# Kernel tuning notes

Hardware: AMD Instinct MI355X
Metric: run time of the kernel (lower is better)

## Reference

```python
import jax, jax.numpy as jnp
import numpy as np

EPS = 1e-6
K = 20
NEG_SLOPE = 0.2

def knn_idx(x, k):
    # x: (B, D, N) flattened vector features; returns (B, N, k) neighbor indices
    inner = -2.0 * jnp.einsum('bdn,bdm->bnm', x, x)
    xx = jnp.sum(x * x, axis=1)  # (B, N)
    pd = -xx[:, :, None] - inner - xx[:, None, :]  # negative squared distance
    _, idx = jax.lax.top_k(pd, k)
    return idx

def get_graph_feature(x, k):
    # x: (B, C, 3, N) -> (B, 2C, 3, N, k) edge features (nbr - ctr, ctr)
    B, C, _, N = x.shape
    idx = knn_idx(x.reshape(B, C * 3, N), k)           # (B, N, k)
    feat = jnp.transpose(x, (0, 3, 1, 2))              # (B, N, C, 3)
    nb = jax.vmap(lambda f, i: f[i])(feat, idx)        # (B, N, k, C, 3)
    ctr = jnp.broadcast_to(feat[:, :, None], nb.shape)
    out = jnp.concatenate([nb - ctr, ctr], axis=3)     # (B, N, k, 2C, 3)
    return jnp.transpose(out, (0, 3, 4, 1, 2))

def vn_batchnorm(x, gamma, beta):
    # x: (B, C, 3, ...); BatchNorm (training stats) applied to vector norms
    norm = jnp.linalg.norm(x, axis=2) + EPS            # (B, C, ...)
    axes = (0,) + tuple(range(2, norm.ndim))
    mu = jnp.mean(norm, axis=axes, keepdims=True)
    var = jnp.var(norm, axis=axes, keepdims=True)
    shape = (1, -1) + (1,) * (norm.ndim - 2)
    nbn = (norm - mu) / jnp.sqrt(var + 1e-5) * gamma.reshape(shape) + beta.reshape(shape)
    return x / norm[:, :, None] * nbn[:, :, None]

def vn_linear_leakyrelu(x, w_feat, w_dir, gamma, beta):
    # x: (B, Cin, 3, ...) -> (B, Cout, 3, ...)
    p = jnp.einsum('oc,bc...->bo...', w_feat, x)
    p = vn_batchnorm(p, gamma, beta)
    d = jnp.einsum('oc,bc...->bo...', w_dir, x)
    dot = jnp.sum(p * d, axis=2, keepdims=True)
    dsq = jnp.sum(d * d, axis=2, keepdims=True)
    proj = p - (dot / (dsq + EPS)) * d
    return NEG_SLOPE * p + (1.0 - NEG_SLOPE) * jnp.where(dot >= 0, p, proj)

def _forward(x, w1, d1, g1, b1, w2, d2, g2, b2, w3, d3, g3, b3, w4, d4, g4, b4, w5, d5, g5, b5):
    h = jnp.transpose(x, (0, 2, 1))[:, None]           # (B, 1, 3, N)
    h = vn_linear_leakyrelu(get_graph_feature(h, K), w1, d1, g1, b1)
    x1 = jnp.mean(h, axis=-1)                          # mean_pool over k: (B, 21, 3, N)
    h = vn_linear_leakyrelu(get_graph_feature(x1, K), w2, d2, g2, b2)
    x2 = jnp.mean(h, axis=-1)                          # (B, 21, 3, N)
    h = vn_linear_leakyrelu(get_graph_feature(x2, K), w3, d3, g3, b3)
    x3 = jnp.mean(h, axis=-1)                          # (B, 42, 3, N)
    h = vn_linear_leakyrelu(get_graph_feature(x3, K), w4, d4, g4, b4)
    x4 = jnp.mean(h, axis=-1)                          # (B, 85, 3, N)
    cat = jnp.concatenate([x1, x2, x3, x4], axis=1)    # (B, 169, 3, N)
    return vn_linear_leakyrelu(cat, w5, d5, g5, b5)    # (B, 341, 3, N)

def setup_inputs():
    key = jax.random.key(0)
    B, N = 8, 1024
    d = {"x": jax.random.normal(key, (B, N, 3), dtype=jnp.float32)}
    feat_shapes = {"1": (21, 2), "2": (21, 42), "3": (42, 42), "4": (85, 84), "5": (341, 169)}
    dir_out = {"1": 21, "2": 21, "3": 42, "4": 85, "5": 1}  # conv5 shares nonlinearity -> 1 dir channel
    for i, (name, (co, ci)) in enumerate(feat_shapes.items()):
        k1, k2 = jax.random.split(jax.random.fold_in(key, i + 1))
        s = 1.0 / np.sqrt(ci)
        d["w" + name] = jax.random.uniform(k1, (co, ci), minval=-s, maxval=s, dtype=jnp.float32)
        d["d" + name] = jax.random.uniform(k2, (dir_out[name], ci), minval=-s, maxval=s, dtype=jnp.float32)
        d["g" + name] = jnp.ones((co,), dtype=jnp.float32)
        d["b" + name] = jnp.zeros((co,), dtype=jnp.float32)
    return d

def reference(x, w1, d1, g1, b1, w2, d2, g2, b2, w3, d3, g3, b3, w4, d4, g4, b4, w5, d5, g5, b5):
    return _forward(x, w1, d1, g1, b1, w2, d2, g2, b2, w3, d3, g3, b3, w4, d4, g4, b4, w5, d5, g5, b5)
```

## Files before the change

### kernel.cpp

```cpp
#include <hip/hip_runtime.h>
#include <math.h>

#define KNN 20
#define NS 0.2f
#define EPSV 1e-6f
#define QT 4
#define OT 8
#define TN 8
#define CROW 507
#define SSPLIT 8

struct F3 { float x, y, z; };

extern __shared__ __align__(16) float smem[];

__global__ void k_transpose(const float* __restrict__ x, float* __restrict__ xt,
                            float* __restrict__ xx, int B, int N) {
    int i = blockIdx.x * blockDim.x + threadIdx.x;
    if (i >= B * N) return;
    int b = i / N, n = i % N;
    const float* src = x + (size_t)(b * N + n) * 3;
    float* dst = xt + (size_t)b * 3 * N + n;
    float s0 = src[0], s1 = src[1], s2 = src[2];
    dst[0] = s0;
    dst[(size_t)N] = s1;
    dst[(size_t)2 * N] = s2;
    float s = 0.f;
    s += s0 * s0;
    s += s1 * s1;
    s += s2 * s2;
    xx[i] = s;
}

__global__ void k_knn_mm(
                         const float* __restrict__ Xn, const float* __restrict__ xx,
                         int* __restrict__ idx, int N, int D,
                         long batchStride, long sliceOff, int qPerBlock,
                         const float* __restrict__ Xp, const float* __restrict__ W,
                         const float* __restrict__ Dw,
                         float* __restrict__ U, float* __restrict__ V,
                         float* __restrict__ UD, float* __restrict__ VD,
                         int C, int Co, int CoP, int TILE,
                         int rowStride, int colOff, int mmBlocks) {
    float* sm = smem;
    int tid = threadIdx.x;

    if ((int)blockIdx.x < mmBlocks) {
        const int CP = C * CoP;
        float* wts = sm;
        float* xs = sm + 4 * CP;
        int bn0 = blockIdx.x * TILE;
        int C3 = C * 3;

        int npad = CoP - Co;
        if (npad) {
            for (int t = tid; t < 4 * C * npad; t += 256) {
                int q = t / npad, oo = Co + t % npad;
                int mat = q / C, c = q % C;
                wts[mat * CP + c * CoP + oo] = 0.f;
            }
        }
        int twoCC = 2 * C * Co;
        for (int t = tid; t < twoCC; t += 256) {
            int o = t / (2 * C), c = t % (2 * C);
            float w = W[t], dw = Dw[t];
            if (c < C) {
                wts[c * CoP + o] = w;
                wts[2 * CP + c * CoP + o] = dw;
            } else {
                wts[CP + (c - C) * CoP + o] = w;
                wts[3 * CP + (c - C) * CoP + o] = dw;
            }
        }
        for (int t = tid; t < TILE * C3; t += 256) {
            int p = t / C3, cc = t % C3;
            xs[t] = Xp[(size_t)(bn0 + p) * rowStride + colOff + cc];
        }
        __syncthreads();
        for (int t = tid; t < CP; t += 256) {
            wts[CP + t] -= wts[t];
            wts[3 * CP + t] -= wts[2 * CP + t];
        }
        __syncthreads();

        int GPP = CoP >> 2;
        int items = TILE * GPP;
        for (int e = tid; e < items; e += 256) {
            int p = e / GPP, og = e - p * GPP;
            int o0 = og * 4;
            const float* xr = xs + p * C3;

            float aU[4][3], aV[4][3], aDu[4][3], aDv[4][3];
#pragma unroll
            for (int i = 0; i < 4; ++i)
#pragma unroll
                for (int j = 0; j < 3; ++j) {
                    aU[i][j] = 0.f; aV[i][j] = 0.f; aDu[i][j] = 0.f; aDv[i][j] = 0.f;
                }

            for (int c = 0; c < C; ++c) {
                float x0 = xr[c * 3], x1 = xr[c * 3 + 1], x2 = xr[c * 3 + 2];
                const float* wp = wts + c * CoP + o0;
                float4 wa4 = *(const float4*)(wp);
                float4 wb4 = *(const float4*)(wp + CP);
                float4 da4 = *(const float4*)(wp + 2 * CP);
                float4 db4 = *(const float4*)(wp + 3 * CP);
                float wav[4] = {wa4.x, wa4.y, wa4.z, wa4.w};
                float wbv[4] = {wb4.x, wb4.y, wb4.z, wb4.w};
                float dav[4] = {da4.x, da4.y, da4.z, da4.w};
                float dbv[4] = {db4.x, db4.y, db4.z, db4.w};
#pragma unroll
                for (int i = 0; i < 4; ++i) {
                    aU[i][0] += wav[i] * x0; aU[i][1] += wav[i] * x1; aU[i][2] += wav[i] * x2;
                    aV[i][0] += wbv[i] * x0; aV[i][1] += wbv[i] * x1; aV[i][2] += wbv[i] * x2;
                    aDu[i][0] += dav[i] * x0; aDu[i][1] += dav[i] * x1; aDu[i][2] += dav[i] * x2;
                    aDv[i][0] += dbv[i] * x0; aDv[i][1] += dbv[i] * x1; aDv[i][2] += dbv[i] * x2;
                }
            }

            size_t base = ((size_t)(bn0 + p) * Co + o0) * 3;
#pragma unroll
            for (int i = 0; i < 4; ++i) {
                int o = o0 + i;
                if (o < Co) {
                    size_t off = base + (size_t)i * 3;
                    U[off] = aU[i][0]; U[off + 1] = aU[i][1]; U[off + 2] = aU[i][2];
                    V[off] = aV[i][0]; V[off + 1] = aV[i][1]; V[off + 2] = aV[i][2];
                    UD[off] = aDu[i][0]; UD[off + 1] = aDu[i][1]; UD[off + 2] = aDu[i][2];
                    VD[off] = aDv[i][0]; VD[off + 1] = aDv[i][1]; VD[off + 2] = aDv[i][2];
                }
            }
        }
        return;
    }

    int kb = (int)blockIdx.x - mmBlocks;
    int qbpb = N / qPerBlock;
    int b = kb / qbpb;
    int qbase = (kb - b * qbpb) * qPerBlock;
    int lane = tid & 63;
    int wave = tid >> 6;

    float* qf = sm;
    float* pdb = sm + 128 * QT;

    const float* Xb = Xn + (size_t)b * batchStride + sliceOff;
    const float* xxb = xx + (size_t)b * N;

    for (int q0 = qbase; q0 < qbase + qPerBlock; q0 += QT) {
        for (int t = tid; t < QT * D; t += 256) {
            int d = t >> 2, q = t & 3;
            qf[d * QT + q] = Xb[(size_t)d * N + (q0 + q)];
        }
        __syncthreads();

        float a0x = 0.f, a0y = 0.f, a0z = 0.f, a0w = 0.f;
        float a1x = 0.f, a1y = 0.f, a1z = 0.f, a1w = 0.f;
        float a2x = 0.f, a2y = 0.f, a2z = 0.f, a2w = 0.f;
        float a3x = 0.f, a3y = 0.f, a3z = 0.f, a3w = 0.f;

        const float* mbase = Xb + 4 * tid;
#pragma unroll 3
        for (int d = 0; d < D; ++d) {
            float4 xm = *(const float4*)(mbase + (size_t)d * N);
            float4 qv = *(const float4*)(qf + d * QT);
            a0x += qv.x * xm.x; a0y += qv.x * xm.y; a0z += qv.x * xm.z; a0w += qv.x * xm.w;
            a1x += qv.y * xm.x; a1y += qv.y * xm.y; a1z += qv.y * xm.z; a1w += qv.y * xm.w;
            a2x += qv.z * xm.x; a2y += qv.z * xm.y; a2z += qv.z * xm.z; a2w += qv.z * xm.w;
            a3x += qv.w * xm.x; a3y += qv.w * xm.y; a3z += qv.w * xm.z; a3w += qv.w * xm.w;
        }

        {
            float4 m2 = *(const float4*)(xxb + 4 * tid);
            float4 qn = *(const float4*)(xxb + q0);
            float4 v;
            v.x = 2.f * a0x - qn.x - m2.x; v.y = 2.f * a0y - qn.x - m2.y;
            v.z = 2.f * a0z - qn.x - m2.z; v.w = 2.f * a0w - qn.x - m2.w;
            *(float4*)(pdb + 0 * 1024 + 4 * tid) = v;
            v.x = 2.f * a1x - qn.y - m2.x; v.y = 2.f * a1y - qn.y - m2.y;
            v.z = 2.f * a1z - qn.y - m2.z; v.w = 2.f * a1w - qn.y - m2.w;
            *(float4*)(pdb + 1 * 1024 + 4 * tid) = v;
            v.x = 2.f * a2x - qn.z - m2.x; v.y = 2.f * a2y - qn.z - m2.y;
            v.z = 2.f * a2z - qn.z - m2.z; v.w = 2.f * a2w - qn.z - m2.w;
            *(float4*)(pdb + 2 * 1024 + 4 * tid) = v;
            v.x = 2.f * a3x - qn.w - m2.x; v.y = 2.f * a3y - qn.w - m2.y;
            v.z = 2.f * a3z - qn.w - m2.z; v.w = 2.f * a3w - qn.w - m2.w;
            *(float4*)(pdb + 3 * 1024 + 4 * tid) = v;
        }
        __syncthreads();

        unsigned long long key[16];
#pragma unroll
        for (int t = 0; t < 16; ++t) {
            unsigned u = __float_as_uint(pdb[wave * 1024 + t * 64 + lane]);
            u ^= (unsigned)((int)u >> 31) | 0x80000000u;
            unsigned lo = (unsigned)(1023 - t * 64) - (unsigned)lane;
            key[t] = ((unsigned long long)u << 32) | (unsigned long long)lo;
        }

#define CE(a, b)                                        \
        {                                               \
            unsigned long long ka = key[a], kb2 = key[b]; \
            bool sw = ka < kb2;                         \
            key[a] = sw ? kb2 : ka;                     \
            key[b] = sw ? ka : kb2;                     \
        }
        CE(0,1) CE(2,3) CE(4,5) CE(6,7) CE(8,9) CE(10,11) CE(12,13) CE(14,15)
        CE(0,2) CE(1,3) CE(4,6) CE(5,7) CE(8,10) CE(9,11) CE(12,14) CE(13,15)
        CE(1,2) CE(5,6) CE(9,10) CE(13,14)
        CE(0,4) CE(1,5) CE(2,6) CE(3,7) CE(8,12) CE(9,13) CE(10,14) CE(11,15)
        CE(2,4) CE(3,5) CE(10,12) CE(11,13)
        CE(1,2) CE(3,4) CE(5,6) CE(9,10) CE(11,12) CE(13,14)
        CE(0,8) CE(1,9) CE(2,10) CE(3,11) CE(4,12) CE(5,13) CE(6,14) CE(7,15)
        CE(4,8) CE(5,9) CE(6,10) CE(7,11)
        CE(2,4) CE(3,5) CE(6,8) CE(7,9) CE(10,12) CE(11,13)
        CE(1,2) CE(3,4) CE(5,6) CE(7,8) CE(9,10) CE(11,12) CE(13,14)
#undef CE

        __syncthreads();
        unsigned long long* kl = (unsigned long long*)(pdb + wave * 1024);
#pragma unroll
        for (int t = 8; t < 16; ++t) kl[(t - 8) * 64 + lane] = key[t];
        int nspill = 0;

        long outBase = ((long)b * N + q0 + wave) * KNN;
        for (int it = 0; it < KNN; ++it) {
            unsigned myh = (unsigned)(key[0] >> 32);
            unsigned mylo = (unsigned)(key[0] & 0xFFFFFFFFull);
            unsigned bh = myh;
#pragma unroll
            for (int off = 32; off >= 1; off >>= 1) {
                unsigned oh = __shfl_xor(bh, off, 64);
                if (oh > bh) bh = oh;
            }
            unsigned long long mask = __ballot(myh == bh);
            unsigned ml;
            if (__popcll(mask) == 1) {
                int src = (int)(__ffsll((long long)mask) - 1);
                ml = __shfl(mylo, src, 64);
            } else {
                unsigned cand = (myh == bh) ? mylo : 0u;
#pragma unroll
                for (int off = 32; off >= 1; off >>= 1) {
                    unsigned oc = __shfl_xor(cand, off, 64);
                    if (oc > cand) cand = oc;
                }
                ml = cand;
            }
            int bi = 1023 - (int)(ml & 1023u);
            if (lane == 0) idx[outBase + it] = bi;
            if ((bi & 63) == lane) {
                key[0] = key[1]; key[1] = key[2]; key[2] = key[3]; key[3] = key[4];
                key[4] = key[5]; key[5] = key[6]; key[6] = key[7];
                int sidx = nspill < 8 ? nspill : 7;
                unsigned long long nv = kl[sidx * 64 + lane];
                key[7] = (nspill < 8) ? nv : 0ull;
                nspill++;
            }
        }
        __syncthreads();
    }
}

__global__ void k_matmul_pair_lds(const float* __restrict__ X, const float* __restrict__ W,
                                  const float* __restrict__ Dw,
                                  float* __restrict__ U, float* __restrict__ V,
                                  float* __restrict__ UD, float* __restrict__ VD,
                                  int C, int Co, int CoP, int TILE,
                                  int rowStride, int colOff) {
    const int CP = C * CoP;
    float* wts = smem;
    float* xs = smem + 4 * CP;

    int tid = threadIdx.x;
    int bn0 = blockIdx.x * TILE;
    int C3 = C * 3;

    int npad = CoP - Co;
    if (npad) {
        for (int t = tid; t < 4 * C * npad; t += 256) {
            int q = t / npad, oo = Co + t % npad;
            int mat = q / C, c = q % C;
            wts[mat * CP + c * CoP + oo] = 0.f;
        }
    }
    int twoCC = 2 * C * Co;
    for (int t = tid; t < twoCC; t += 256) {
        int o = t / (2 * C), c = t % (2 * C);
        float w = W[t], dw = Dw[t];
        if (c < C) {
            wts[c * CoP + o] = w;
            wts[2 * CP + c * CoP + o] = dw;
        } else {
            wts[CP + (c - C) * CoP + o] = w;
            wts[3 * CP + (c - C) * CoP + o] = dw;
        }
    }
    for (int t = tid; t < TILE * C3; t += 256) {
        int p = t / C3, cc = t % C3;
        xs[t] = X[(size_t)(bn0 + p) * rowStride + colOff + cc];
    }
    __syncthreads();
    for (int t = tid; t < CP; t += 256) {
        wts[CP + t] -= wts[t];
        wts[3 * CP + t] -= wts[2 * CP + t];
    }
    __syncthreads();

    int GPP = CoP >> 2;
    int items = TILE * GPP;
    for (int e = tid; e < items; e += 256) {
        int p = e / GPP, og = e - p * GPP;
        int o0 = og * 4;
        const float* xr = xs + p * C3;

        float aU[4][3], aV[4][3], aDu[4][3], aDv[4][3];
#pragma unroll
        for (int i = 0; i < 4; ++i)
#pragma unroll
            for (int j = 0; j < 3; ++j) {
                aU[i][j] = 0.f; aV[i][j] = 0.f; aDu[i][j] = 0.f; aDv[i][j] = 0.f;
            }

        for (int c = 0; c < C; ++c) {
            float x0 = xr[c * 3], x1 = xr[c * 3 + 1], x2 = xr[c * 3 + 2];
            const float* wp = wts + c * CoP + o0;
            float4 wa4 = *(const float4*)(wp);
            float4 wb4 = *(const float4*)(wp + CP);
            float4 da4 = *(const float4*)(wp + 2 * CP);
            float4 db4 = *(const float4*)(wp + 3 * CP);
            float wav[4] = {wa4.x, wa4.y, wa4.z, wa4.w};
            float wbv[4] = {wb4.x, wb4.y, wb4.z, wb4.w};
            float dav[4] = {da4.x, da4.y, da4.z, da4.w};
            float dbv[4] = {db4.x, db4.y, db4.z, db4.w};
#pragma unroll
            for (int i = 0; i < 4; ++i) {
                aU[i][0] += wav[i] * x0; aU[i][1] += wav[i] * x1; aU[i][2] += wav[i] * x2;
                aV[i][0] += wbv[i] * x0; aV[i][1] += wbv[i] * x1; aV[i][2] += wbv[i] * x2;
                aDu[i][0] += dav[i] * x0; aDu[i][1] += dav[i] * x1; aDu[i][2] += dav[i] * x2;
                aDv[i][0] += dbv[i] * x0; aDv[i][1] += dbv[i] * x1; aDv[i][2] += dbv[i] * x2;
            }
        }

        size_t base = ((size_t)(bn0 + p) * Co + o0) * 3;
#pragma unroll
        for (int i = 0; i < 4; ++i) {
            int o = o0 + i;
            if (o < Co) {
                size_t off = base + (size_t)i * 3;
                U[off] = aU[i][0]; U[off + 1] = aU[i][1]; U[off + 2] = aU[i][2];
                V[off] = aV[i][0]; V[off + 1] = aV[i][1]; V[off + 2] = aV[i][2];
                UD[off] = aDu[i][0]; UD[off + 1] = aDu[i][1]; UD[off + 2] = aDu[i][2];
                VD[off] = aDv[i][0]; VD[off + 1] = aDv[i][1]; VD[off + 2] = aDv[i][2];
            }
        }
    }
}

__global__ void k_stats_edge_det(const float* __restrict__ U, const float* __restrict__ V,
                                 const int* __restrict__ idx, float* __restrict__ partials,
                                 int N, int Co, int BN) {
    int o = blockIdx.x;
    int s = blockIdx.y;
    int tid = threadIdx.x;
    int P = BN / SSPLIT;
    int g0 = s * P;

    __shared__ float Ush[3072];
    __shared__ float r1[256], r2[256];

    for (int t = tid; t < P; t += 256) {
        F3 u3 = *(const F3*)(U + ((size_t)(g0 + t) * Co + o) * 3);
        Ush[t * 3 + 0] = u3.x;
        Ush[t * 3 + 1] = u3.y;
        Ush[t * 3 + 2] = u3.z;
    }
    __syncthreads();

    float s1 = 0.f, s2 = 0.f;
    for (int pl = tid; pl < P; pl += 256) {
        int g = g0 + pl;
        F3 v3 = *(const F3*)(V + ((size_t)g * Co + o) * 3);
        float v0 = v3.x, v1 = v3.y, v2 = v3.z;
        const int* ip = idx + (size_t)g * KNN;
        for (int kk = 0; kk < KNN; ++kk) {
            const float* Ur = Ush + ip[kk] * 3;
            float p0 = Ur[0] + v0;
            float p1 = Ur[1] + v1;
            float p2 = Ur[2] + v2;
            float nm = sqrtf(p0 * p0 + p1 * p1 + p2 * p2) + EPSV;
            s1 += nm;
            s2 += nm * nm;
        }
    }
    r1[tid] = s1; r2[tid] = s2;
    __syncthreads();
    for (int st = 128; st > 0; st >>= 1) {
        if (tid < st) { r1[tid] += r1[tid + st]; r2[tid] += r2[tid + st]; }
        __syncthreads();
    }
    if (tid == 0) {
        partials[(o * SSPLIT + s) * 2] = r1[0];
        partials[(o * SSPLIT + s) * 2 + 1] = r2[0];
    }
}

__global__ void k_final_fused(const float* __restrict__ U, const float* __restrict__ V,
                              const float* __restrict__ UD, const float* __restrict__ VD,
                              const int* __restrict__ idx, const float* __restrict__ partials,
                              const float* __restrict__ gamma, const float* __restrict__ beta,
                              float* __restrict__ catp, float* __restrict__ catn,
                              float* __restrict__ xx,
                              int N, int Co, int colOff, float cnt, int doSq) {
    int b = blockIdx.y;
    int n0 = blockIdx.x * TN;
    int tid = threadIdx.x;
    int CC = Co * 3;

    __shared__ float tile[TN * 255];
    __shared__ float muS[85], invS[85];

    for (int o = tid; o < Co; o += 256) {
        float s1 = 0.f, s2 = 0.f;
        for (int s = 0; s < SSPLIT; ++s) {
            s1 += partials[(o * SSPLIT + s) * 2];
            s2 += partials[(o * SSPLIT + s) * 2 + 1];
        }
        float mu = s1 / cnt;
        float var = s2 / cnt - mu * mu;
        muS[o] = mu;
        invS[o] = rsqrtf(var + 1e-5f);
    }
    __syncthreads();

    const float invk = 1.f / (float)KNN;
    int items = TN * Co;
    for (int e = tid; e < items; e += 256) {
        int nl = e / Co, o = e - nl * Co;
        int n = n0 + nl;
        float mu = muS[o], inv = invS[o];
        float gmm = gamma[o], bt = beta[o];

        size_t ctr = ((size_t)(b * N + n) * Co + o) * 3;
        F3 vc = *(const F3*)(V + ctr);
        F3 wc = *(const F3*)(VD + ctr);
        float v0 = vc.x, v1 = vc.y, v2 = vc.z;
        float w0 = wc.x, w1 = wc.y, w2 = wc.z;
        const int* ip = idx + ((size_t)b * N + n) * KNN;

        float a0 = 0.f, a1 = 0.f, a2 = 0.f;
        for (int kk = 0; kk < KNN; ++kk) {
            int m = ip[kk];
            size_t nb = ((size_t)(b * N + m) * Co + o) * 3;
            F3 un = *(const F3*)(U + nb);
            F3 dn = *(const F3*)(UD + nb);
            float p0 = un.x + v0;
            float p1 = un.y + v1;
            float p2 = un.z + v2;
            float nm = sqrtf(p0 * p0 + p1 * p1 + p2 * p2) + EPSV;
            float nbn = (nm - mu) * inv * gmm + bt;
            float sc = nbn / nm;
            p0 *= sc; p1 *= sc; p2 *= sc;
            float d0 = dn.x + w0;
            float d1 = dn.y + w1;
            float d2 = dn.z + w2;
            float dot = p0 * d0 + p1 * d1 + p2 * d2;
            if (dot >= 0.f) {
                a0 += p0; a1 += p1; a2 += p2;
            } else {
                float f = dot / (d0 * d0 + d1 * d1 + d2 * d2 + EPSV);
                a0 += NS * p0 + (1.f - NS) * (p0 - f * d0);
                a1 += NS * p1 + (1.f - NS) * (p1 - f * d1);
                a2 += NS * p2 + (1.f - NS) * (p2 - f * d2);
            }
        }
        tile[nl * CC + o * 3 + 0] = a0 * invk;
        tile[nl * CC + o * 3 + 1] = a1 * invk;
        tile[nl * CC + o * 3 + 2] = a2 * invk;
    }
    __syncthreads();

    for (int t = tid; t < TN * CC; t += 256) {
        int nl = t / CC, c = t - nl * CC;
        catp[(size_t)(b * N + n0 + nl) * CROW + colOff + c] = tile[nl * CC + c];
    }
    for (int t = tid; t < TN * CC; t += 256) {
        int c = t >> 3, nl = t & (TN - 1);
        catn[(size_t)b * CROW * N + (size_t)(colOff + c) * N + n0 + nl] = tile[nl * CC + c];
    }
    if (doSq && tid < TN) {
        const float* row = tile + tid * CC;
        float s = 0.f;
        for (int c = 0; c < CC; ++c) {
            float v = row[c];
            s += v * v;
        }
        xx[(size_t)b * N + n0 + tid] = s;
    }
}

__global__ void k_matmul_plain(const float* __restrict__ X, const float* __restrict__ W,
                               const float* __restrict__ Dw,
                               float* __restrict__ U, float* __restrict__ Ud,
                               int N, int Cin, int Cout, long batchStride, long sliceOff) {
    int ot = blockIdx.y;
    int b = blockIdx.z;
    int tid = threadIdx.x;
    int n = blockIdx.x * 512 + 2 * tid;

    const float* Wp; float* Up; int CoutE; int o0;
    if (ot == (int)gridDim.y - 1) {
        Wp = Dw; Up = Ud; CoutE = 1; o0 = 0;
    } else {
        Wp = W; Up = U; CoutE = Cout; o0 = ot * OT;
    }

    __shared__ __align__(16) float wsm[OT][176];
    for (int t = tid; t < OT * Cin; t += 256) {
        int oo = t / Cin, c = t % Cin;
        int o = o0 + oo;
        wsm[oo][c] = (o < CoutE) ? Wp[(size_t)o * Cin + c] : 0.f;
    }
    __syncthreads();

    const float* Xp = X + (size_t)b * batchStride + sliceOff + n;
    float au[OT][3][2];
#pragma unroll
    for (int oo = 0; oo < OT; ++oo)
#pragma unroll
        for (int j = 0; j < 3; ++j) {
            au[oo][j][0] = 0.f; au[oo][j][1] = 0.f;
        }

    int c = 0;
    for (; c + 4 <= Cin; c += 4) {
        float2 xv[4][3];
#pragma unroll
        for (int cc = 0; cc < 4; ++cc)
#pragma unroll
            for (int j = 0; j < 3; ++j)
                xv[cc][j] = *(const float2*)(Xp + ((size_t)(c + cc) * 3 + j) * N);
#pragma unroll
        for (int oo = 0; oo < OT; ++oo) {
            float4 w4 = *(const float4*)&wsm[oo][c];
            float wv[4] = {w4.x, w4.y, w4.z, w4.w};
#pragma unroll
            for (int j = 0; j < 3; ++j) {
#pragma unroll
                for (int cc = 0; cc < 4; ++cc) {
                    au[oo][j][0] += wv[cc] * xv[cc][j].x;
                    au[oo][j][1] += wv[cc] * xv[cc][j].y;
                }
            }
        }
    }
    for (; c < Cin; ++c) {
        float2 xv[3];
#pragma unroll
        for (int j = 0; j < 3; ++j)
            xv[j] = *(const float2*)(Xp + ((size_t)c * 3 + j) * N);
#pragma unroll
        for (int oo = 0; oo < OT; ++oo) {
            float wv = wsm[oo][c];
#pragma unroll
            for (int j = 0; j < 3; ++j) {
                au[oo][j][0] += wv * xv[j].x;
                au[oo][j][1] += wv * xv[j].y;
            }
        }
    }
#pragma unroll
    for (int oo = 0; oo < OT; ++oo) {
        int o = o0 + oo;
        if (o < CoutE) {
#pragma unroll
            for (int j = 0; j < 3; ++j) {
                float2 st; st.x = au[oo][j][0]; st.y = au[oo][j][1];
                *(float2*)&Up[(((size_t)b * CoutE + o) * 3 + j) * N + n] = st;
            }
        }
    }
}

__global__ void k_stats_plain_det(const float* __restrict__ U, float* __restrict__ mv,
                                  int N, int Cout, int BN, float cnt) {
    int o = blockIdx.x;
    int tid = threadIdx.x;
    float s1 = 0.f, s2 = 0.f;
    for (int g = tid; g < BN; g += 256) {
        int b = g / N, n = g % N;
        const float* Ub = U + (((size_t)b * Cout + o) * 3) * N;
        float p0 = Ub[n], p1 = Ub[(size_t)N + n], p2 = Ub[(size_t)2 * N + n];
        float nm = sqrtf(p0 * p0 + p1 * p1 + p2 * p2) + EPSV;
        s1 += nm;
        s2 += nm * nm;
    }
    __shared__ float r1[256], r2[256];
    r1[tid] = s1; r2[tid] = s2;
    __syncthreads();
    for (int st = 128; st > 0; st >>= 1) {
        if (tid < st) { r1[tid] += r1[tid + st]; r2[tid] += r2[tid + st]; }
        __syncthreads();
    }
    if (tid == 0) {
        float mu = r1[0] / cnt;
        float var = r2[0] / cnt - mu * mu;
        mv[2 * o] = mu;
        mv[2 * o + 1] = rsqrtf(var + 1e-5f);
    }
}

__global__ void k_final_plain(const float* __restrict__ U, const float* __restrict__ Dv,
                              const float* __restrict__ mv,
                              const float* __restrict__ gamma, const float* __restrict__ beta,
                              float* __restrict__ out, int N, int Cout) {
    int b = blockIdx.z, o = blockIdx.y, tid = threadIdx.x;
    int n = blockIdx.x * 256 + tid;
    float mu = mv[2 * o];
    float inv = mv[2 * o + 1];
    float g = gamma[o], bt = beta[o];

    const float* Ub = U + (((size_t)b * Cout + o) * 3) * N;
    float p0 = Ub[n], p1 = Ub[(size_t)N + n], p2 = Ub[(size_t)2 * N + n];
    float nm = sqrtf(p0 * p0 + p1 * p1 + p2 * p2) + EPSV;
    float nbn = (nm - mu) * inv * g + bt;
    float sc = nbn / nm;
    p0 *= sc; p1 *= sc; p2 *= sc;

    float d0 = Dv[((size_t)b * 3 + 0) * N + n];
    float d1 = Dv[((size_t)b * 3 + 1) * N + n];
    float d2 = Dv[((size_t)b * 3 + 2) * N + n];
    float dot = p0 * d0 + p1 * d1 + p2 * d2;
    float o0, o1, o2;
    if (dot >= 0.f) {
        o0 = p0; o1 = p1; o2 = p2;
    } else {
        float f = dot / (d0 * d0 + d1 * d1 + d2 * d2 + EPSV);
        o0 = NS * p0 + (1.f - NS) * (p0 - f * d0);
        o1 = NS * p1 + (1.f - NS) * (p1 - f * d1);
        o2 = NS * p2 + (1.f - NS) * (p2 - f * d2);
    }
    size_t ob = (((size_t)b * Cout + o) * 3) * N + n;
    out[ob] = o0;
    out[ob + (size_t)N] = o1;
    out[ob + (size_t)2 * N] = o2;
}

extern "C" void kernel_launch(void* const* d_in, const int* in_sizes, int n_in,
                              void* d_out, int out_size, void* d_ws, size_t ws_size,
                              hipStream_t stream) {
    (void)in_sizes; (void)n_in; (void)out_size; (void)ws_size;
    const int B = 8, N = 1024;

    const float* x = (const float*)d_in[0];
    const float* W[5]; const float* Dw[5]; const float* G[5]; const float* Bt[5];
    for (int l = 0; l < 5; ++l) {
        W[l]  = (const float*)d_in[1 + 4 * l];
        Dw[l] = (const float*)d_in[2 + 4 * l];
        G[l]  = (const float*)d_in[3 + 4 * l];
        Bt[l] = (const float*)d_in[4 + 4 * l];
    }

    float* ws = (float*)d_ws;
    size_t off = 0;
    float* xt = ws + off;     off += (size_t)B * 3 * N;
    int* idx = (int*)(ws + off); off += (size_t)B * N * KNN;
    float* catp = ws + off;   off += (size_t)B * N * CROW;
    float* catn = ws + off;   off += (size_t)B * N * CROW;
    float* Up = ws + off;     off += (size_t)B * N * 85 * 3;
    float* Vp = ws + off;     off += (size_t)B * N * 85 * 3;
    float* UDp = ws + off;    off += (size_t)B * N * 85 * 3;
    float* VDp = ws + off;    off += (size_t)B * N * 85 * 3;
    float* U5 = ws + off;     off += (size_t)B * 341 * 3 * N;
    float* d5buf = ws + off;  off += (size_t)B * 3 * N;
    float* xx = ws + off;     off += (size_t)B * N;
    float* partials = ws + off; off += (size_t)341 * SSPLIT * 2;
    float* mv = ws + off;     off += 2 * 341;

    k_transpose<<<(B * N + 255) / 256, 256, 0, stream>>>(x, xt, xx, B, N);

    const int Cin_[4]  = {1, 21, 21, 42};
    const int Cout_[4] = {21, 21, 42, 85};
    const int inOff_[4] = {-1, 0, 21, 42};
    const int outOff_[4] = {0, 21, 42, 84};
    const int Tile_[4] = {32, 32, 16, 8};

    const int BN = B * N;
    const size_t KNN_LDS = (size_t)(128 * QT + QT * 1024) * sizeof(float);

    for (int l = 0; l < 4; ++l) {
        int C = Cin_[l], Co = Cout_[l];
        int D = C * 3;
        int CoP = (Co + 3) & ~3;
        int TILE = Tile_[l];

        const float* Xn; long bs, so;
        if (inOff_[l] < 0) { Xn = xt; bs = (long)3 * N; so = 0; }
        else { Xn = catn; bs = (long)CROW * N; so = (long)inOff_[l] * 3 * N; }

        const float* Xp; int rs, co;
        if (inOff_[l] < 0) { Xp = x; rs = 3; co = 0; }
        else { Xp = catp; rs = CROW; co = inOff_[l] * 3; }

        size_t mmNeed = (size_t)(4 * C * CoP + TILE * C * 3) * sizeof(float);

        if (l < 3) {
            int mmB = BN / TILE;
            int knnB = BN / 8;
            size_t smemB = mmNeed > KNN_LDS ? mmNeed : KNN_LDS;
            k_knn_mm<<<mmB + knnB, 256, smemB, stream>>>(
                Xn, xx, idx, N, D, bs, so, 8,
                Xp, W[l], Dw[l], Up, Vp, UDp, VDp, C, Co, CoP, TILE, rs, co, mmB);
        } else {
            k_knn_mm<<<BN / 4, 256, KNN_LDS, stream>>>(
                Xn, xx, idx, N, D, bs, so, 4,
                Xp, W[l], Dw[l], Up, Vp, UDp, VDp, C, Co, CoP, TILE, rs, co, 0);
            k_matmul_pair_lds<<<BN / TILE, 256, mmNeed, stream>>>(
                Xp, W[l], Dw[l], Up, Vp, UDp, VDp, C, Co, CoP, TILE, rs, co);
        }

        dim3 gst(Co, SSPLIT);
        k_stats_edge_det<<<gst, 256, 0, stream>>>(Up, Vp, idx, partials, N, Co, BN);

        int doSq = (l < 3) ? 1 : 0;
        dim3 gf(N / TN, B);
        k_final_fused<<<gf, 256, 0, stream>>>(
            Up, Vp, UDp, VDp, idx, partials, G[l], Bt[l],
            catp, catn, xx, N, Co, outOff_[l] * 3,
            (float)((size_t)BN * KNN), doSq);
    }

    {
        long bs = (long)CROW * N, so = 0;
        dim3 gm5(N / 512, (341 + OT - 1) / OT + 1, B);
        k_matmul_plain<<<gm5, 256, 0, stream>>>(catn, W[4], Dw[4], U5, d5buf,
                                                N, 169, 341, bs, so);
        k_stats_plain_det<<<341, 256, 0, stream>>>(U5, mv, N, 341, BN, (float)BN);
        dim3 gs5(N / 256, 341, B);
        k_final_plain<<<gs5, 256, 0, stream>>>(U5, d5buf, mv, G[4], Bt[4],
                                               (float*)d_out, N, 341);
    }
}
```

Before: 653.1 us.

## Fuse layer-4 matmul into kNN kernel via output-channel-chunked weight staging

Layer 4 now runs its pairwise matmul inside the combined kNN/matmul launch instead of a separate kernel. To keep LDS usage at the kNN level, weights are staged 12 output channels at a time and the matmul loops over chunks. The kNN part for this layer now uses 8 queries per block like the other layers. This removes a launch and lets matmul overlap with kNN, at the cost of extra barriers and low thread utilisation per chunk.

```diff
diff --git a/kernel.cpp b/kernel.cpp
--- a/kernel.cpp
+++ b/kernel.cpp
@@ -7,6 +7,7 @@
 #define QT 4
 #define OT 8
 #define TN 8
+#define OCH 12
 #define CROW 507
 #define SSPLIT 8
 
@@ -41,93 +42,167 @@
                          float* __restrict__ U, float* __restrict__ V,
                          float* __restrict__ UD, float* __restrict__ VD,
                          int C, int Co, int CoP, int TILE,
-                         int rowStride, int colOff, int mmBlocks) {
+                         int rowStride, int colOff, int mmBlocks, int chunked) {
     float* sm = smem;
     int tid = threadIdx.x;
 
     if ((int)blockIdx.x < mmBlocks) {
-        const int CP = C * CoP;
-        float* wts = sm;
-        float* xs = sm + 4 * CP;
+        int C3 = C * 3;
         int bn0 = blockIdx.x * TILE;
-        int C3 = C * 3;
-
-        int npad = CoP - Co;
-        if (npad) {
-            for (int t = tid; t < 4 * C * npad; t += 256) {
-                int q = t / npad, oo = Co + t % npad;
-                int mat = q / C, c = q % C;
-                wts[mat * CP + c * CoP + oo] = 0.f;
-            }
-        }
-        int twoCC = 2 * C * Co;
-        for (int t = tid; t < twoCC; t += 256) {
-            int o = t / (2 * C), c = t % (2 * C);
-            float w = W[t], dw = Dw[t];
-            if (c < C) {
-                wts[c * CoP + o] = w;
-                wts[2 * CP + c * CoP + o] = dw;
-            } else {
-                wts[CP + (c - C) * CoP + o] = w;
-                wts[3 * CP + (c - C) * CoP + o] = dw;
-            }
-        }
-        for (int t = tid; t < TILE * C3; t += 256) {
-            int p = t / C3, cc = t % C3;
-            xs[t] = Xp[(size_t)(bn0 + p) * rowStride + colOff + cc];
-        }
-        __syncthreads();
-        for (int t = tid; t < CP; t += 256) {
-            wts[CP + t] -= wts[t];
-            wts[3 * CP + t] -= wts[2 * CP + t];
-        }
-        __syncthreads();
-
-        int GPP = CoP >> 2;
-        int items = TILE * GPP;
-        for (int e = tid; e < items; e += 256) {
-            int p = e / GPP, og = e - p * GPP;
-            int o0 = og * 4;
-            const float* xr = xs + p * C3;
-
-            float aU[4][3], aV[4][3], aDu[4][3], aDv[4][3];
-#pragma unroll
-            for (int i = 0; i < 4; ++i)
-#pragma unroll
-                for (int j = 0; j < 3; ++j) {
-                    aU[i][j] = 0.f; aV[i][j] = 0.f; aDu[i][j] = 0.f; aDv[i][j] = 0.f;
-                }
-
-            for (int c = 0; c < C; ++c) {
-                float x0 = xr[c * 3], x1 = xr[c * 3 + 1], x2 = xr[c * 3 + 2];
-                const float* wp = wts + c * CoP + o0;
-                float4 wa4 = *(const float4*)(wp);
-                float4 wb4 = *(const float4*)(wp + CP);
-                float4 da4 = *(const float4*)(wp + 2 * CP);
-                float4 db4 = *(const float4*)(wp + 3 * CP);
-                float wav[4] = {wa4.x, wa4.y, wa4.z, wa4.w};
-                float wbv[4] = {wb4.x, wb4.y, wb4.z, wb4.w};
-                float dav[4] = {da4.x, da4.y, da4.z, da4.w};
-                float dbv[4] = {db4.x, db4.y, db4.z, db4.w};
+        if (!chunked) {
+            const int CP = C * CoP;
+            float* wts = sm;
+            float* xs = sm + 4 * CP;
+
+            int npad = CoP - Co;
+            if (npad) {
+                for (int t = tid; t < 4 * C * npad; t += 256) {
+                    int q = t / npad, oo = Co + t % npad;
+                    int mat = q / C, c = q % C;
+                    wts[mat * CP + c * CoP + oo] = 0.f;
+                }
+            }
+            int twoCC = 2 * C * Co;
+            for (int t = tid; t < twoCC; t += 256) {
+                int o = t / (2 * C), c = t % (2 * C);
+                float w = W[t], dw = Dw[t];
+                if (c < C) {
+                    wts[c * CoP + o] = w;
+                    wts[2 * CP + c * CoP + o] = dw;
+                } else {
+                    wts[CP + (c - C) * CoP + o] = w;
+                    wts[3 * CP + (c - C) * CoP + o] = dw;
+                }
+            }
+            for (int t = tid; t < TILE * C3; t += 256) {
+                int p = t / C3, cc = t % C3;
+                xs[t] = Xp[(size_t)(bn0 + p) * rowStride + colOff + cc];
+            }
+            __syncthreads();
+            for (int t = tid; t < CP; t += 256) {
+                wts[CP + t] -= wts[t];
+                wts[3 * CP + t] -= wts[2 * CP + t];
+            }
+            __syncthreads();
+
+            int GPP = CoP >> 2;
+            int items = TILE * GPP;
+            for (int e = tid; e < items; e += 256) {
+                int p = e / GPP, og = e - p * GPP;
+                int o0 = og * 4;
+                const float* xr = xs + p * C3;
+
+                float aU[4][3], aV[4][3], aDu[4][3], aDv[4][3];
+#pragma unroll
+                for (int i = 0; i < 4; ++i)
+#pragma unroll
+                    for (int j = 0; j < 3; ++j) {
+                        aU[i][j] = 0.f; aV[i][j] = 0.f; aDu[i][j] = 0.f; aDv[i][j] = 0.f;
+                    }
+
+                for (int c = 0; c < C; ++c) {
+                    float x0 = xr[c * 3], x1 = xr[c * 3 + 1], x2 = xr[c * 3 + 2];
+                    const float* wp = wts + c * CoP + o0;
+                    float4 wa4 = *(const float4*)(wp);
+                    float4 wb4 = *(const float4*)(wp + CP);
+                    float4 da4 = *(const float4*)(wp + 2 * CP);
+                    float4 db4 = *(const float4*)(wp + 3 * CP);
+                    float wav[4] = {wa4.x, wa4.y, wa4.z, wa4.w};
+                    float wbv[4] = {wb4.x, wb4.y, wb4.z, wb4.w};
+                    float dav[4] = {da4.x, da4.y, da4.z, da4.w};
+                    float dbv[4] = {db4.x, db4.y, db4.z, db4.w};
+#pragma unroll
+                    for (int i = 0; i < 4; ++i) {
+                        aU[i][0] += wav[i] * x0; aU[i][1] += wav[i] * x1; aU[i][2] += wav[i] * x2;
+                        aV[i][0] += wbv[i] * x0; aV[i][1] += wbv[i] * x1; aV[i][2] += wbv[i] * x2;
+                        aDu[i][0] += dav[i] * x0; aDu[i][1] += dav[i] * x1; aDu[i][2] += dav[i] * x2;
+                        aDv[i][0] += dbv[i] * x0; aDv[i][1] += dbv[i] * x1; aDv[i][2] += dbv[i] * x2;
+                    }
+                }
+
+                size_t base = ((size_t)(bn0 + p) * Co + o0) * 3;
 #pragma unroll
                 for (int i = 0; i < 4; ++i) {
-                    aU[i][0] += wav[i] * x0; aU[i][1] += wav[i] * x1; aU[i][2] += wav[i] * x2;
-                    aV[i][0] += wbv[i] * x0; aV[i][1] += wbv[i] * x1; aV[i][2] += wbv[i] * x2;
-                    aDu[i][0] += dav[i] * x0; aDu[i][1] += dav[i] * x1; aDu[i][2] += dav[i] * x2;
-                    aDv[i][0] += dbv[i] * x0; aDv[i][1] += dbv[i] * x1; aDv[i][2] += dbv[i] * x2;
-                }
-            }
-
-            size_t base = ((size_t)(bn0 + p) * Co + o0) * 3;
-#pragma unroll
-            for (int i = 0; i < 4; ++i) {
-                int o = o0 + i;
-                if (o < Co) {
-                    size_t off = base + (size_t)i * 3;
-                    U[off] = aU[i][0]; U[off + 1] = aU[i][1]; U[off + 2] = aU[i][2];
-                    V[off] = aV[i][0]; V[off + 1] = aV[i][1]; V[off + 2] = aV[i][2];
-                    UD[off] = aDu[i][0]; UD[off + 1] = aDu[i][1]; UD[off + 2] = aDu[i][2];
-                    VD[off] = aDv[i][0]; VD[off + 1] = aDv[i][1]; VD[off + 2] = aDv[i][2];
+                    int o = o0 + i;
+                    if (o < Co) {
+                        size_t off = base + (size_t)i * 3;
+                        U[off] = aU[i][0]; U[off + 1] = aU[i][1]; U[off + 2] = aU[i][2];
+                        V[off] = aV[i][0]; V[off + 1] = aV[i][1]; V[off + 2] = aV[i][2];
+                        UD[off] = aDu[i][0]; UD[off + 1] = aDu[i][1]; UD[off + 2] = aDu[i][2];
+                        VD[off] = aDv[i][0]; VD[off + 1] = aDv[i][1]; VD[off + 2] = aDv[i][2];
+                    }
+                }
+            }
+        } else {
+            float* xs = sm + 4 * (C * OCH);
+            for (int t = tid; t < TILE * C3; t += 256) {
+                int p = t / C3, cc = t % C3;
+                xs[t] = Xp[(size_t)(bn0 + p) * rowStride + colOff + cc];
+            }
+            for (int o0c = 0; o0c < CoP; o0c += OCH) {
+                int och = CoP - o0c; if (och > OCH) och = OCH;
+                int CPc = C * och;
+                float* wts = sm;
+                __syncthreads();
+                for (int t = tid; t < 4 * CPc; t += 256) {
+                    int mat = t / CPc; int r = t - mat * CPc;
+                    int c = r / och; int oo = r - c * och;
+                    int o = o0c + oo;
+                    const float* srcw = (mat < 2) ? W : Dw;
+                    int cc = (mat & 1) ? (C + c) : c;
+                    wts[mat * CPc + c * och + oo] =
+                        (o < Co) ? srcw[(size_t)o * 2 * C + cc] : 0.f;
+                }
+                __syncthreads();
+                for (int t = tid; t < CPc; t += 256) {
+                    wts[CPc + t] -= wts[t];
+                    wts[3 * CPc + t] -= wts[2 * CPc + t];
+                }
+                __syncthreads();
+                int GPP = och >> 2;
+                int items = TILE * GPP;
+                for (int e = tid; e < items; e += 256) {
+                    int p = e / GPP, og = e - p * GPP;
+                    int o0 = og * 4;
+                    const float* xr = xs + p * C3;
+                    float aU[4][3], aV[4][3], aDu[4][3], aDv[4][3];
+#pragma unroll
+                    for (int i = 0; i < 4; ++i)
+#pragma unroll
+                        for (int j = 0; j < 3; ++j) {
+                            aU[i][j] = 0.f; aV[i][j] = 0.f; aDu[i][j] = 0.f; aDv[i][j] = 0.f;
+                        }
+                    for (int c = 0; c < C; ++c) {
+                        float x0 = xr[c * 3], x1 = xr[c * 3 + 1], x2 = xr[c * 3 + 2];
+                        const float* wp = wts + c * och + o0;
+                        float4 wa4 = *(const float4*)(wp);
+                        float4 wb4 = *(const float4*)(wp + CPc);
+                        float4 da4 = *(const float4*)(wp + 2 * CPc);
+                        float4 db4 = *(const float4*)(wp + 3 * CPc);
+                        float wav[4] = {wa4.x, wa4.y, wa4.z, wa4.w};
+                        float wbv[4] = {wb4.x, wb4.y, wb4.z, wb4.w};
+                        float dav[4] = {da4.x, da4.y, da4.z, da4.w};
+                        float dbv[4] = {db4.x, db4.y, db4.z, db4.w};
+#pragma unroll
+                        for (int i = 0; i < 4; ++i) {
+                            aU[i][0] += wav[i] * x0; aU[i][1] += wav[i] * x1; aU[i][2] += wav[i] * x2;
+                            aV[i][0] += wbv[i] * x0; aV[i][1] += wbv[i] * x1; aV[i][2] += wbv[i] * x2;
+                            aDu[i][0] += dav[i] * x0; aDu[i][1] += dav[i] * x1; aDu[i][2] += dav[i] * x2;
+                            aDv[i][0] += dbv[i] * x0; aDv[i][1] += dbv[i] * x1; aDv[i][2] += dbv[i] * x2;
+                        }
+                    }
+                    size_t base = ((size_t)(bn0 + p) * Co + (o0c + o0)) * 3;
+#pragma unroll
+                    for (int i = 0; i < 4; ++i) {
+                        int o = o0c + o0 + i;
+                        if (o < Co) {
+                            size_t off = base + (size_t)i * 3;
+                            U[off] = aU[i][0]; U[off + 1] = aU[i][1]; U[off + 2] = aU[i][2];
+                            V[off] = aV[i][0]; V[off + 1] = aV[i][1]; V[off + 2] = aV[i][2];
+                            UD[off] = aDu[i][0]; UD[off + 1] = aDu[i][1]; UD[off + 2] = aDu[i][2];
+                            VD[off] = aDv[i][0]; VD[off + 1] = aDv[i][1]; VD[off + 2] = aDv[i][2];
+                        }
+                    }
                 }
             }
         }
@@ -259,101 +334,6 @@
             }
         }
         __syncthreads();
-    }
-}
-
-__global__ void k_matmul_pair_lds(const float* __restrict__ X, const float* __restrict__ W,
-                                  const float* __restrict__ Dw,
-                                  float* __restrict__ U, float* __restrict__ V,
-                                  float* __restrict__ UD, float* __restrict__ VD,
-                                  int C, int Co, int CoP, int TILE,
-                                  int rowStride, int colOff) {
-    const int CP = C * CoP;
-    float* wts = smem;
-    float* xs = smem + 4 * CP;
-
-    int tid = threadIdx.x;
-    int bn0 = blockIdx.x * TILE;
-    int C3 = C * 3;
-
-    int npad = CoP - Co;
-    if (npad) {
-        for (int t = tid; t < 4 * C * npad; t += 256) {
-            int q = t / npad, oo = Co + t % npad;
-            int mat = q / C, c = q % C;
-            wts[mat * CP + c * CoP + oo] = 0.f;
-        }
-    }
-    int twoCC = 2 * C * Co;
-    for (int t = tid; t < twoCC; t += 256) {
-        int o = t / (2 * C), c = t % (2 * C);
-        float w = W[t], dw = Dw[t];
-        if (c < C) {
-            wts[c * CoP + o] = w;
-            wts[2 * CP + c * CoP + o] = dw;
-        } else {
-            wts[CP + (c - C) * CoP + o] = w;
-            wts[3 * CP + (c - C) * CoP + o] = dw;
-        }
-    }
-    for (int t = tid; t < TILE * C3; t += 256) {
-        int p = t / C3, cc = t % C3;
-        xs[t] = X[(size_t)(bn0 + p) * rowStride + colOff + cc];
-    }
-    __syncthreads();
-    for (int t = tid; t < CP; t += 256) {
-        wts[CP + t] -= wts[t];
-        wts[3 * CP + t] -= wts[2 * CP + t];
-    }
-    __syncthreads();
-
-    int GPP = CoP >> 2;
-    int items = TILE * GPP;
-    for (int e = tid; e < items; e += 256) {
-        int p = e / GPP, og = e - p * GPP;
-        int o0 = og * 4;
-        const float* xr = xs + p * C3;
-
-        float aU[4][3], aV[4][3], aDu[4][3], aDv[4][3];
-#pragma unroll
-        for (int i = 0; i < 4; ++i)
-#pragma unroll
-            for (int j = 0; j < 3; ++j) {
-                aU[i][j] = 0.f; aV[i][j] = 0.f; aDu[i][j] = 0.f; aDv[i][j] = 0.f;
-            }
-
-        for (int c = 0; c < C; ++c) {
-            float x0 = xr[c * 3], x1 = xr[c * 3 + 1], x2 = xr[c * 3 + 2];
-            const float* wp = wts + c * CoP + o0;
-            float4 wa4 = *(const float4*)(wp);
-            float4 wb4 = *(const float4*)(wp + CP);
-            float4 da4 = *(const float4*)(wp + 2 * CP);
-            float4 db4 = *(const float4*)(wp + 3 * CP);
-            float wav[4] = {wa4.x, wa4.y, wa4.z, wa4.w};
-            float wbv[4] = {wb4.x, wb4.y, wb4.z, wb4.w};
-            float dav[4] = {da4.x, da4.y, da4.z, da4.w};
-            float dbv[4] = {db4.x, db4.y, db4.z, db4.w};
-#pragma unroll
-            for (int i = 0; i < 4; ++i) {
-                aU[i][0] += wav[i] * x0; aU[i][1] += wav[i] * x1; aU[i][2] += wav[i] * x2;
-                aV[i][0] += wbv[i] * x0; aV[i][1] += wbv[i] * x1; aV[i][2] += wbv[i] * x2;
-                aDu[i][0] += dav[i] * x0; aDu[i][1] += dav[i] * x1; aDu[i][2] += dav[i] * x2;
-                aDv[i][0] += dbv[i] * x0; aDv[i][1] += dbv[i] * x1; aDv[i][2] += dbv[i] * x2;
-            }
-        }
-
-        size_t base = ((size_t)(bn0 + p) * Co + o0) * 3;
-#pragma unroll
-        for (int i = 0; i < 4; ++i) {
-            int o = o0 + i;
-            if (o < Co) {
-                size_t off = base + (size_t)i * 3;
-                U[off] = aU[i][0]; U[off + 1] = aU[i][1]; U[off + 2] = aU[i][2];
-                V[off] = aV[i][0]; V[off + 1] = aV[i][1]; V[off + 2] = aV[i][2];
-                UD[off] = aDu[i][0]; UD[off + 1] = aDu[i][1]; UD[off + 2] = aDu[i][2];
-                VD[off] = aDv[i][0]; VD[off + 1] = aDv[i][1]; VD[off + 2] = aDv[i][2];
-            }
-        }
     }
 }
 
@@ -693,6 +673,7 @@
         int D = C * 3;
         int CoP = (Co + 3) & ~3;
         int TILE = Tile_[l];
+        int chunked = (l == 3) ? 1 : 0;
 
         const float* Xn; long bs, so;
         if (inOff_[l] < 0) { Xn = xt; bs = (long)3 * N; so = 0; }
@@ -702,22 +683,15 @@
         if (inOff_[l] < 0) { Xp = x; rs = 3; co = 0; }
         else { Xp = catp; rs = CROW; co = inOff_[l] * 3; }
 
-        size_t mmNeed = (size_t)(4 * C * CoP + TILE * C * 3) * sizeof(float);
-
-        if (l < 3) {
-            int mmB = BN / TILE;
-            int knnB = BN / 8;
-            size_t smemB = mmNeed > KNN_LDS ? mmNeed : KNN_LDS;
-            k_knn_mm<<<mmB + knnB, 256, smemB, stream>>>(
-                Xn, xx, idx, N, D, bs, so, 8,
-                Xp, W[l], Dw[l], Up, Vp, UDp, VDp, C, Co, CoP, TILE, rs, co, mmB);
-        } else {
-            k_knn_mm<<<BN / 4, 256, KNN_LDS, stream>>>(
-                Xn, xx, idx, N, D, bs, so, 4,
-                Xp, W[l], Dw[l], Up, Vp, UDp, VDp, C, Co, CoP, TILE, rs, co, 0);
-            k_matmul_pair_lds<<<BN / TILE, 256, mmNeed, stream>>>(
-                Xp, W[l], Dw[l], Up, Vp, UDp, VDp, C, Co, CoP, TILE, rs, co);
-        }
+        int mmB = BN / TILE;
+        int knnB = BN / 8;
+        size_t mmNeed = chunked
+            ? (size_t)(4 * C * OCH + TILE * C * 3) * sizeof(float)
+            : (size_t)(4 * C * CoP + TILE * C * 3) * sizeof(float);
+        size_t smemB = mmNeed > KNN_LDS ? mmNeed : KNN_LDS;
+        k_knn_mm<<<mmB + knnB, 256, smemB, stream>>>(
+            Xn, xx, idx, N, D, bs, so, 8,
+            Xp, W[l], Dw[l], Up, Vp, UDp, VDp, C, Co, CoP, TILE, rs, co, mmB, chunked);
 
         dim3 gst(Co, SSPLIT);
         k_stats_edge_det<<<gst, 256, 0, stream>>>(Up, Vp, idx, partials, N, Co, BN);
```

New measurement: 672.7 us. +3.0%, slower.
